# Optimization experiments

Hardware: AMD Instinct MI355X
Metric: run time of the kernel (lower is better)

Reference implementation:

```python
import jax, jax.numpy as jnp
import numpy as np

B, S, E = 8, 2048, 768


def setup_inputs() -> dict:
    key = jax.random.key(0)
    ks = jax.random.split(key, 9)
    scale = 1.0 / np.sqrt(E)
    return {
        "value": jax.random.normal(ks[0], (B, S, E), jnp.float32),
        "key": jax.random.normal(ks[1], (B, S, E), jnp.float32),
        "query": jax.random.normal(ks[2], (B, S, E), jnp.float32),
        "mask": jax.random.randint(ks[3], (B, 1, S), 0, 2, jnp.int32),
        "Wv": jax.random.normal(ks[4], (E, E), jnp.float32) * scale,
        "Wk": jax.random.normal(ks[5], (E, E), jnp.float32) * scale,
        "Wq": jax.random.normal(ks[6], (E, E), jnp.float32) * scale,
        "Wo": jax.random.normal(ks[7], (E, E), jnp.float32) * scale,
        "bo": jax.random.normal(ks[8], (E,), jnp.float32) * 0.01,
    }


def reference(value, key, query, mask, Wv, Wk, Wq, Wo, bo):
    # nn.Linear: y = x @ W.T  (no bias for v/k/q)
    v = jnp.einsum('bse,oe->bso', value, Wv)
    k = jnp.einsum('bse,oe->bso', key, Wk)
    q = jnp.einsum('bse,oe->bso', query, Wq)
    inv_sqrt_e = 1.0 / jnp.sqrt(jnp.float32(E))
    # NOTE: original divides BOTH q and k by sqrt(E) -> effective 1/E scaling
    q = q * inv_sqrt_e
    k = k * inv_sqrt_e
    scores = jnp.einsum('bqe,bke->bqk', q, k)  # [B, S, S]
    scores = jnp.where(mask == 0, -jnp.inf, scores)
    attn = jax.nn.softmax(scores, axis=-1)
    out = jnp.einsum('bqk,bke->bqe', attn, v)
    out = jnp.einsum('bse,oe->bso', out, Wo) + bo
    return out
```

## Files before the change

### kernel.cpp

```cpp
#include <hip/hip_runtime.h>
#include <hip/hip_bf16.h>
#include <stdint.h>

#define E_DIM 768
#define S_LEN 2048
#define BATCH 8

typedef __attribute__((ext_vector_type(8))) short short8;
typedef __attribute__((ext_vector_type(4))) float floatx4;

__device__ __forceinline__ short f2bf(float f) {
    return __builtin_bit_cast(short, __float2bfloat16(f));
}

__device__ __forceinline__ floatx4 mfma16(short8 a, short8 b, floatx4 c) {
    return __builtin_amdgcn_mfma_f32_16x16x32_bf16(a, b, c, 0, 0, 0);
}

__device__ __forceinline__ void glds16(const short* g, short* l) {
    __builtin_amdgcn_global_load_lds(
        (const __attribute__((address_space(1))) void*)g,
        (__attribute__((address_space(3))) void*)l,
        16, 0, 0);
}

__device__ __forceinline__ void gemm_core(
    const short* __restrict__ Abase, size_t sA,
    const short* __restrict__ Bbase, size_t sB,
    int K,
    short* At, short* Bt,
    floatx4 acc[4][4])
{
    const int tid  = threadIdx.x;
    const int lane = tid & 63;
    const int wv   = tid >> 6;
    const int lm   = lane & 15, lq = lane >> 4;
    const int rl   = lane >> 3, sl = lane & 7;
    const int usw  = sl ^ rl;
    const int wm   = (wv & 1) * 64, wn = (wv >> 1) * 64;

    const short* ag = Abase + (size_t)(wv * 32 + rl) * sA + usw * 8;
    const short* bg = Bbase + (size_t)(wv * 32 + rl) * sB + usw * 8;
    short* al = At + wv * 4 * 512;
    short* bl = Bt + wv * 4 * 512;
    const size_t askip = 8 * sA, bskip = 8 * sB;

    for (int kt = 0; kt < K; kt += 64) {
#pragma unroll
        for (int c = 0; c < 4; ++c) glds16(ag + c * askip + kt, al + c * 512);
#pragma unroll
        for (int c = 0; c < 4; ++c) glds16(bg + c * bskip + kt, bl + c * 512);
        __syncthreads();

#pragma unroll
        for (int s = 0; s < 2; ++s) {
            const int u = s * 4 + lq;
            short8 af[4], bf[4];
#pragma unroll
            for (int i = 0; i < 4; ++i) {
                int r = wm + i * 16 + lm;
                af[i] = *(const short8*)&At[((r >> 3) * 64 + (r & 7) * 8 + (u ^ (r & 7))) * 8];
            }
#pragma unroll
            for (int j = 0; j < 4; ++j) {
                int r = wn + j * 16 + lm;
                bf[j] = *(const short8*)&Bt[((r >> 3) * 64 + (r & 7) * 8 + (u ^ (r & 7))) * 8];
            }
#pragma unroll
            for (int i = 0; i < 4; ++i)
#pragma unroll
                for (int j = 0; j < 4; ++j)
                    acc[i][j] = mfma16(af[i], bf[j], acc[i][j]);
        }
        __syncthreads();
    }
}

__global__ void mask_scan(const int* __restrict__ mask, int* __restrict__ jidx,
                          int* __restrict__ nv, int* __restrict__ nvp) {
    const int b = blockIdx.x;
    const int t = threadIdx.x;
    __shared__ int cnt[256];
    int m[8];
    int c = 0;
#pragma unroll
    for (int k = 0; k < 8; ++k) {
        m[k] = mask[b * S_LEN + t * 8 + k];
        c += (m[k] != 0);
    }
    cnt[t] = c;
    __syncthreads();
    for (int off = 1; off < 256; off <<= 1) {
        int v = (t >= off) ? cnt[t - off] : 0;
        __syncthreads();
        cnt[t] += v;
        __syncthreads();
    }
    int pos = cnt[t] - c;
    const int total = cnt[255];
#pragma unroll
    for (int k = 0; k < 8; ++k)
        if (m[k] != 0) jidx[b * S_LEN + (pos++)] = t * 8 + k;
    __syncthreads();
    for (int i = total + t; i < S_LEN; i += 256) jidx[b * S_LEN + i] = 0;
    if (t == 0) {
        nv[b] = total;
        int p = (total + 127) & ~127;
        if (p < 128) p = 128;
        nvp[b] = p;
    }
}

__global__ void convert_gather(const float* __restrict__ v, const float* __restrict__ k,
                               const float* __restrict__ q,
                               const int* __restrict__ jidx, const int* __restrict__ nvp,
                               short* __restrict__ xv, short* __restrict__ xk,
                               short* __restrict__ xq) {
    const int z = blockIdx.y, b = blockIdx.z;
    const int r0 = blockIdx.x * 4;
    if (z < 2 && r0 >= nvp[b]) return;
    const float* src = (z == 0) ? v : (z == 1) ? k : q;
    short* dst = (z == 0) ? xv : (z == 1) ? xk : xq;
    const int tid = threadIdx.x;
#pragma unroll
    for (int p = 0; p < 3; ++p) {
        int g   = p * 256 + tid;
        int row = r0 + g / 192;
        int c4  = (g % 192) * 4;
        int srow = (z == 2) ? row : jidx[b * S_LEN + row];
        float4 f = *(const float4*)(src + ((size_t)b * S_LEN + srow) * E_DIM + c4);
        short4 h;
        h.x = f2bf(f.x); h.y = f2bf(f.y); h.z = f2bf(f.z); h.w = f2bf(f.w);
        *(short4*)(dst + ((size_t)b * S_LEN + row) * E_DIM + c4) = h;
    }
}

__global__ void convert_wts(const float* __restrict__ wv, const float* __restrict__ wk,
                            const float* __restrict__ wq, const float* __restrict__ wo,
                            short* __restrict__ o) {
    const int z = blockIdx.y;
    const float* src = (z == 0) ? wv : (z == 1) ? wk : (z == 2) ? wq : wo;
    const float scale = (z == 2) ? (1.0f / (float)E_DIM) : 1.0f;
    size_t i = ((size_t)blockIdx.x * 256 + threadIdx.x) * 4;
    float4 f = *(const float4*)(src + i);
    short4 h;
    h.x = f2bf(f.x * scale); h.y = f2bf(f.y * scale);
    h.z = f2bf(f.z * scale); h.w = f2bf(f.w * scale);
    *(short4*)(o + (size_t)z * E_DIM * E_DIM + i) = h;
}

__global__ __launch_bounds__(256, 3) void proj_kernel(
    const short* __restrict__ xv, const short* __restrict__ xk, const short* __restrict__ xq,
    const short* __restrict__ Wb, const int* __restrict__ nvp,
    short* __restrict__ vt, short* __restrict__ kb, short* __restrict__ qb)
{
    const int z  = blockIdx.z;
    const int mt = blockIdx.x;
    const int n0 = blockIdx.y * 128;

    int b = 0, lm0 = 0;
    const short* X;
    if (z == 2) {
        X = xq + (size_t)mt * 128 * E_DIM;
    } else {
        b   = mt >> 4;
        lm0 = (mt & 15) * 128;
        if (lm0 >= nvp[b]) return;
        X = ((z == 0) ? xv : xk) + ((size_t)b * S_LEN + lm0) * E_DIM;
    }
    const short* W = Wb + (size_t)z * E_DIM * E_DIM + (size_t)n0 * E_DIM;

    __shared__ short At[128 * 64];
    __shared__ short Bt[128 * 64];

    floatx4 acc[4][4];
#pragma unroll
    for (int i = 0; i < 4; ++i)
#pragma unroll
        for (int j = 0; j < 4; ++j) acc[i][j] = (floatx4){0.f, 0.f, 0.f, 0.f};

    gemm_core(X, E_DIM, W, E_DIM, E_DIM, At, Bt, acc);

    const int lane = threadIdx.x & 63, wv = threadIdx.x >> 6;
    const int lm = lane & 15, lq = lane >> 4;
    const int wm = (wv & 1) * 64, wn = (wv >> 1) * 64;

    if (z == 0) {
#pragma unroll
        for (int i = 0; i < 4; ++i)
#pragma unroll
            for (int r = 0; r < 4; ++r) {
                int li = lm0 + wm + i * 16 + lq * 4 + r;
#pragma unroll
                for (int j = 0; j < 4; ++j) {
                    int n = n0 + wn + j * 16 + lm;
                    vt[((size_t)b * E_DIM + n) * S_LEN + li] = f2bf(acc[i][j][r]);
                }
            }
    } else if (z == 1) {
#pragma unroll
        for (int i = 0; i < 4; ++i)
#pragma unroll
            for (int r = 0; r < 4; ++r) {
                int li = lm0 + wm + i * 16 + lq * 4 + r;
#pragma unroll
                for (int j = 0; j < 4; ++j) {
                    int n = n0 + wn + j * 16 + lm;
                    kb[((size_t)b * S_LEN + li) * E_DIM + n] = f2bf(acc[i][j][r]);
                }
            }
    } else {
#pragma unroll
        for (int i = 0; i < 4; ++i)
#pragma unroll
            for (int r = 0; r < 4; ++r) {
                int m = mt * 128 + wm + i * 16 + lq * 4 + r;
#pragma unroll
                for (int j = 0; j < 4; ++j) {
                    int n = n0 + wn + j * 16 + lm;
                    qb[(size_t)m * E_DIM + n] = f2bf(acc[i][j][r]);
                }
            }
    }
}

__global__ __launch_bounds__(256, 3) void score_kernel(
    const short* __restrict__ qb, const short* __restrict__ kb,
    const int* __restrict__ nv, const int* __restrict__ nvp,
    short* __restrict__ P, float* __restrict__ rowsum)
{
    const int b  = blockIdx.z;
    const int m0 = blockIdx.x * 128;
    const int n0 = blockIdx.y * 128;
    if (n0 >= nvp[b]) return;

    __shared__ short At[128 * 64];
    __shared__ short Bt[128 * 64];

    floatx4 acc[4][4];
#pragma unroll
    for (int i = 0; i < 4; ++i)
#pragma unroll
        for (int j = 0; j < 4; ++j) acc[i][j] = (floatx4){0.f, 0.f, 0.f, 0.f};

    gemm_core(qb + ((size_t)b * S_LEN + m0) * E_DIM, E_DIM,
              kb + ((size_t)b * S_LEN + n0) * E_DIM, E_DIM, E_DIM, At, Bt, acc);

    const int lane = threadIdx.x & 63, wv = threadIdx.x >> 6;
    const int lm = lane & 15, lq = lane >> 4;
    const int wm = (wv & 1) * 64, wn = (wv >> 1) * 64;
    const int nvb = nv[b];

    float rsum[4][4];
#pragma unroll
    for (int i = 0; i < 4; ++i)
#pragma unroll
        for (int r = 0; r < 4; ++r) rsum[i][r] = 0.f;

    const size_t Pbb = (size_t)b * S_LEN * S_LEN;
#pragma unroll
    for (int j = 0; j < 4; ++j) {
        int n = n0 + wn + j * 16 + lm;
        bool valid = n < nvb;
#pragma unroll
        for (int i = 0; i < 4; ++i) {
            int mbase = m0 + wm + i * 16 + lq * 4;
#pragma unroll
            for (int r = 0; r < 4; ++r) {
                float p = valid ? __expf(acc[i][j][r]) : 0.0f;
                rsum[i][r] += p;
                P[Pbb + (size_t)(mbase + r) * S_LEN + n] = f2bf(p);
            }
        }
    }
#pragma unroll
    for (int i = 0; i < 4; ++i)
#pragma unroll
        for (int r = 0; r < 4; ++r) {
            float v = rsum[i][r];
            v += __shfl_xor(v, 1);
            v += __shfl_xor(v, 2);
            v += __shfl_xor(v, 4);
            v += __shfl_xor(v, 8);
            if (lm == 0)
                atomicAdd(&rowsum[b * S_LEN + m0 + wm + i * 16 + lq * 4 + r], v);
        }
}

__global__ __launch_bounds__(256, 3) void pv_kernel(
    const short* __restrict__ P, const short* __restrict__ vt,
    const float* __restrict__ rowsum, const int* __restrict__ nvp,
    short* __restrict__ abuf)
{
    const int b  = blockIdx.z;
    const int m0 = blockIdx.x * 128;
    const int n0 = blockIdx.y * 128;

    __shared__ short At[128 * 64];
    __shared__ short Bt[128 * 64];

    floatx4 acc[4][4];
#pragma unroll
    for (int i = 0; i < 4; ++i)
#pragma unroll
        for (int j = 0; j < 4; ++j) acc[i][j] = (floatx4){0.f, 0.f, 0.f, 0.f};

    gemm_core(P + (size_t)b * S_LEN * S_LEN + (size_t)m0 * S_LEN, S_LEN,
              vt + ((size_t)b * E_DIM + n0) * S_LEN, S_LEN, nvp[b], At, Bt, acc);

    const int lane = threadIdx.x & 63, wv = threadIdx.x >> 6;
    const int lm = lane & 15, lq = lane >> 4;
    const int wm = (wv & 1) * 64, wn = (wv >> 1) * 64;

#pragma unroll
    for (int i = 0; i < 4; ++i) {
        int mbase = m0 + wm + i * 16 + lq * 4;
#pragma unroll
        for (int r = 0; r < 4; ++r) {
            float inv = 1.0f / rowsum[b * S_LEN + mbase + r];
            size_t ob = ((size_t)b * S_LEN + mbase + r) * E_DIM;
#pragma unroll
            for (int j = 0; j < 4; ++j) {
                int n = n0 + wn + j * 16 + lm;
                abuf[ob + n] = f2bf(acc[i][j][r] * inv);
            }
        }
    }
}

__global__ __launch_bounds__(256, 3) void out_kernel(
    const short* __restrict__ A, const short* __restrict__ W,
    const float* __restrict__ bias, float* __restrict__ Y)
{
    const int m0 = blockIdx.x * 128;
    const int n0 = blockIdx.y * 128;

    __shared__ short At[128 * 64];
    __shared__ short Bt[128 * 64];

    floatx4 acc[4][4];
#pragma unroll
    for (int i = 0; i < 4; ++i)
#pragma unroll
        for (int j = 0; j < 4; ++j) acc[i][j] = (floatx4){0.f, 0.f, 0.f, 0.f};

    gemm_core(A + (size_t)m0 * E_DIM, E_DIM, W + (size_t)n0 * E_DIM, E_DIM,
              E_DIM, At, Bt, acc);

    const int lane = threadIdx.x & 63, wv = threadIdx.x >> 6;
    const int lm = lane & 15, lq = lane >> 4;
    const int wm = (wv & 1) * 64, wn = (wv >> 1) * 64;

#pragma unroll
    for (int j = 0; j < 4; ++j) {
        int n = n0 + wn + j * 16 + lm;
        float bv = bias[n];
#pragma unroll
        for (int i = 0; i < 4; ++i)
#pragma unroll
            for (int r = 0; r < 4; ++r) {
                int m = m0 + wm + i * 16 + lq * 4 + r;
                Y[(size_t)m * E_DIM + n] = acc[i][j][r] + bv;
            }
    }
}

extern "C" void kernel_launch(void* const* d_in, const int* in_sizes, int n_in,
                              void* d_out, int out_size, void* d_ws, size_t ws_size,
                              hipStream_t stream) {
    const float* value = (const float*)d_in[0];
    const float* key   = (const float*)d_in[1];
    const float* query = (const float*)d_in[2];
    const int*   mask  = (const int*)d_in[3];
    const float* Wv    = (const float*)d_in[4];
    const float* Wk    = (const float*)d_in[5];
    const float* Wq    = (const float*)d_in[6];
    const float* Wo    = (const float*)d_in[7];
    const float* bo    = (const float*)d_in[8];
    float* out = (float*)d_out;

    const size_t WN  = (size_t)E_DIM * E_DIM;
    const size_t ACT = (size_t)BATCH * S_LEN * E_DIM;

    short* Wb  = (short*)d_ws;
    short* xv  = Wb + 4 * WN;
    short* xk  = xv + ACT;
    short* xq  = xk + ACT;
    short* vt  = xq + ACT;
    short* kb  = vt + ACT;
    short* qb  = kb + ACT;
    float* rowsum = (float*)(qb + ACT);
    int*   nv  = (int*)(rowsum + (size_t)BATCH * S_LEN);
    int*   nvp = nv + BATCH;
    int*   jidx = (int*)qb;
    short* P    = xv;
    short* abuf = qb;

    hipMemsetAsync(rowsum, 0, (size_t)BATCH * S_LEN * sizeof(float), stream);

    mask_scan<<<BATCH, 256, 0, stream>>>(mask, jidx, nv, nvp);
    convert_wts<<<dim3(576, 4), 256, 0, stream>>>(Wv, Wk, Wq, Wo, Wb);
    convert_gather<<<dim3(512, 3, 8), 256, 0, stream>>>(value, key, query,
                                                        jidx, nvp, xv, xk, xq);

    proj_kernel<<<dim3(128, 6, 3), 256, 0, stream>>>(xv, xk, xq, Wb, nvp,
                                                     vt, kb, qb);

    score_kernel<<<dim3(16, 16, 8), 256, 0, stream>>>(qb, kb, nv, nvp, P, rowsum);

    pv_kernel<<<dim3(16, 6, 8), 256, 0, stream>>>(P, vt, rowsum, nvp, abuf);

    out_kernel<<<dim3(128, 6), 256, 0, stream>>>(abuf, Wb + 3 * WN, bo, out);
}
```

Measured before the change: 347.3 us.

## Stage GEMM epilogues through padded LDS tile for coalesced 16-byte global stores

The proj, score and pv kernels now write their bf16 output tiles into a padded shared-memory buffer (stride 132), then copy it to global memory with 16-byte vector stores per thread. Before, each thread stored scattered 2-byte elements, and the V-transpose store was badly strided. The shared buffer reuses the A/B staging space, and launch bounds change from 3 to 4 waves-per-SIMD occupancy. The cost is an extra barrier and LDS round trip, plus register pressure under the tighter occupancy bound.

Measured after the change: 381.0 us. 9.7% more time.

```diff
diff --git a/kernel.cpp b/kernel.cpp
--- a/kernel.cpp
+++ b/kernel.cpp
@@ -5,6 +5,7 @@
 #define E_DIM 768
 #define S_LEN 2048
 #define BATCH 8
+#define CT_STRIDE 132
 
 typedef __attribute__((ext_vector_type(8))) short short8;
 typedef __attribute__((ext_vector_type(4))) float floatx4;
@@ -76,6 +77,47 @@
     }
 }
 
+__device__ __forceinline__ void acc_to_ct(floatx4 acc[4][4], short* Ct) {
+    const int lane = threadIdx.x & 63, wv = threadIdx.x >> 6;
+    const int lm = lane & 15, lq = lane >> 4;
+    const int wm = (wv & 1) * 64, wn = (wv >> 1) * 64;
+#pragma unroll
+    for (int i = 0; i < 4; ++i)
+#pragma unroll
+        for (int j = 0; j < 4; ++j)
+#pragma unroll
+            for (int r = 0; r < 4; ++r)
+                Ct[(wm + i * 16 + lq * 4 + r) * CT_STRIDE + wn + j * 16 + lm] =
+                    f2bf(acc[i][j][r]);
+}
+
+__device__ __forceinline__ void acc_to_ct_T(floatx4 acc[4][4], short* Ct) {
+    const int lane = threadIdx.x & 63, wv = threadIdx.x >> 6;
+    const int lm = lane & 15, lq = lane >> 4;
+    const int wm = (wv & 1) * 64, wn = (wv >> 1) * 64;
+#pragma unroll
+    for (int i = 0; i < 4; ++i)
+#pragma unroll
+        for (int j = 0; j < 4; ++j) {
+            short4 h;
+            h.x = f2bf(acc[i][j][0]); h.y = f2bf(acc[i][j][1]);
+            h.z = f2bf(acc[i][j][2]); h.w = f2bf(acc[i][j][3]);
+            *(short4*)&Ct[(wn + j * 16 + lm) * CT_STRIDE + wm + i * 16 + lq * 4] = h;
+        }
+}
+
+__device__ __forceinline__ void ct_writeback(const short* Ct, short* dst,
+                                             size_t dstride) {
+    __syncthreads();
+    const int tid = threadIdx.x;
+    const int row = tid >> 1, half = tid & 1;
+    const short* src = Ct + row * CT_STRIDE + half * 64;
+    short* d = dst + (size_t)row * dstride + half * 64;
+#pragma unroll
+    for (int u = 0; u < 8; ++u)
+        *(uint4*)(d + u * 8) = *(const uint4*)(src + u * 8);
+}
+
 __global__ void mask_scan(const int* __restrict__ mask, int* __restrict__ jidx,
                           int* __restrict__ nv, int* __restrict__ nvp) {
     const int b = blockIdx.x;
@@ -149,7 +191,7 @@
     *(short4*)(o + (size_t)z * E_DIM * E_DIM + i) = h;
 }
 
-__global__ __launch_bounds__(256, 3) void proj_kernel(
+__global__ __launch_bounds__(256, 4) void proj_kernel(
     const short* __restrict__ xv, const short* __restrict__ xk, const short* __restrict__ xq,
     const short* __restrict__ Wb, const int* __restrict__ nvp,
     short* __restrict__ vt, short* __restrict__ kb, short* __restrict__ qb)
@@ -170,8 +212,9 @@
     }
     const short* W = Wb + (size_t)z * E_DIM * E_DIM + (size_t)n0 * E_DIM;
 
-    __shared__ short At[128 * 64];
-    __shared__ short Bt[128 * 64];
+    __shared__ short smem[128 * CT_STRIDE];
+    short* At = smem;
+    short* Bt = smem + 8192;
 
     floatx4 acc[4][4];
 #pragma unroll
@@ -181,50 +224,19 @@
 
     gemm_core(X, E_DIM, W, E_DIM, E_DIM, At, Bt, acc);
 
-    const int lane = threadIdx.x & 63, wv = threadIdx.x >> 6;
-    const int lm = lane & 15, lq = lane >> 4;
-    const int wm = (wv & 1) * 64, wn = (wv >> 1) * 64;
-
     if (z == 0) {
-#pragma unroll
-        for (int i = 0; i < 4; ++i)
-#pragma unroll
-            for (int r = 0; r < 4; ++r) {
-                int li = lm0 + wm + i * 16 + lq * 4 + r;
-#pragma unroll
-                for (int j = 0; j < 4; ++j) {
-                    int n = n0 + wn + j * 16 + lm;
-                    vt[((size_t)b * E_DIM + n) * S_LEN + li] = f2bf(acc[i][j][r]);
-                }
-            }
+        acc_to_ct_T(acc, smem);
+        ct_writeback(smem, vt + ((size_t)b * E_DIM + n0) * S_LEN + lm0, S_LEN);
     } else if (z == 1) {
-#pragma unroll
-        for (int i = 0; i < 4; ++i)
-#pragma unroll
-            for (int r = 0; r < 4; ++r) {
-                int li = lm0 + wm + i * 16 + lq * 4 + r;
-#pragma unroll
-                for (int j = 0; j < 4; ++j) {
-                    int n = n0 + wn + j * 16 + lm;
-                    kb[((size_t)b * S_LEN + li) * E_DIM + n] = f2bf(acc[i][j][r]);
-                }
-            }
+        acc_to_ct(acc, smem);
+        ct_writeback(smem, kb + ((size_t)b * S_LEN + lm0) * E_DIM + n0, E_DIM);
     } else {
-#pragma unroll
-        for (int i = 0; i < 4; ++i)
-#pragma unroll
-            for (int r = 0; r < 4; ++r) {
-                int m = mt * 128 + wm + i * 16 + lq * 4 + r;
-#pragma unroll
-                for (int j = 0; j < 4; ++j) {
-                    int n = n0 + wn + j * 16 + lm;
-                    qb[(size_t)m * E_DIM + n] = f2bf(acc[i][j][r]);
-                }
-            }
-    }
-}
-
-__global__ __launch_bounds__(256, 3) void score_kernel(
+        acc_to_ct(acc, smem);
+        ct_writeback(smem, qb + (size_t)mt * 128 * E_DIM + n0, E_DIM);
+    }
+}
+
+__global__ __launch_bounds__(256, 4) void score_kernel(
     const short* __restrict__ qb, const short* __restrict__ kb,
     const int* __restrict__ nv, const int* __restrict__ nvp,
     short* __restrict__ P, float* __restrict__ rowsum)
@@ -234,8 +246,9 @@
     const int n0 = blockIdx.y * 128;
     if (n0 >= nvp[b]) return;
 
-    __shared__ short At[128 * 64];
-    __shared__ short Bt[128 * 64];
+    __shared__ short smem[128 * CT_STRIDE];
+    short* At = smem;
+    short* Bt = smem + 8192;
 
     floatx4 acc[4][4];
 #pragma unroll
@@ -257,22 +270,23 @@
 #pragma unroll
         for (int r = 0; r < 4; ++r) rsum[i][r] = 0.f;
 
-    const size_t Pbb = (size_t)b * S_LEN * S_LEN;
 #pragma unroll
     for (int j = 0; j < 4; ++j) {
-        int n = n0 + wn + j * 16 + lm;
-        bool valid = n < nvb;
-#pragma unroll
-        for (int i = 0; i < 4; ++i) {
-            int mbase = m0 + wm + i * 16 + lq * 4;
+        bool valid = (n0 + wn + j * 16 + lm) < nvb;
+#pragma unroll
+        for (int i = 0; i < 4; ++i)
 #pragma unroll
             for (int r = 0; r < 4; ++r) {
                 float p = valid ? __expf(acc[i][j][r]) : 0.0f;
+                acc[i][j][r] = p;
                 rsum[i][r] += p;
-                P[Pbb + (size_t)(mbase + r) * S_LEN + n] = f2bf(p);
             }
-        }
-    }
+    }
+
+    acc_to_ct(acc, smem);
+    ct_writeback(smem, P + (size_t)b * S_LEN * S_LEN + (size_t)m0 * S_LEN + n0,
+                 S_LEN);
+
 #pragma unroll
     for (int i = 0; i < 4; ++i)
 #pragma unroll
@@ -287,7 +301,7 @@
         }
 }
 
-__global__ __launch_bounds__(256, 3) void pv_kernel(
+__global__ __launch_bounds__(256, 4) void pv_kernel(
     const short* __restrict__ P, const short* __restrict__ vt,
     const float* __restrict__ rowsum, const int* __restrict__ nvp,
     short* __restrict__ abuf)
@@ -296,8 +310,9 @@
     const int m0 = blockIdx.x * 128;
     const int n0 = blockIdx.y * 128;
 
-    __shared__ short At[128 * 64];
-    __shared__ short Bt[128 * 64];
+    __shared__ short smem[128 * CT_STRIDE];
+    short* At = smem;
+    short* Bt = smem + 8192;
 
     floatx4 acc[4][4];
 #pragma unroll
@@ -309,8 +324,8 @@
               vt + ((size_t)b * E_DIM + n0) * S_LEN, S_LEN, nvp[b], At, Bt, acc);
 
     const int lane = threadIdx.x & 63, wv = threadIdx.x >> 6;
-    const int lm = lane & 15, lq = lane >> 4;
-    const int wm = (wv & 1) * 64, wn = (wv >> 1) * 64;
+    const int lq = lane >> 4;
+    const int wm = (wv & 1) * 64;
 
 #pragma unroll
     for (int i = 0; i < 4; ++i) {
@@ -318,14 +333,13 @@
 #pragma unroll
         for (int r = 0; r < 4; ++r) {
             float inv = 1.0f / rowsum[b * S_LEN + mbase + r];
-            size_t ob = ((size_t)b * S_LEN + mbase + r) * E_DIM;
-#pragma unroll
-            for (int j = 0; j < 4; ++j) {
-                int n = n0 + wn + j * 16 + lm;
-                abuf[ob + n] = f2bf(acc[i][j][r] * inv);
-            }
+#pragma unroll
+            for (int j = 0; j < 4; ++j) acc[i][j][r] *= inv;
         }
     }
+
+    acc_to_ct(acc, smem);
+    ct_writeback(smem, abuf + ((size_t)b * S_LEN + m0) * E_DIM + n0, E_DIM);
 }
 
 __global__ __launch_bounds__(256, 3) void out_kernel(
```
